# Performance work log

Hardware: AMD Instinct MI355X
Metric: run time of the kernel (lower is better)

Reference implementation:

```python
import jax, jax.numpy as jnp
import numpy as np

N, E, FN, FE, H, B = 8192, 32768, 32, 16, 73, 64
T_MP, T_S2S = 3, 12


def setup_inputs() -> dict:
    key = jax.random.key(0)
    k = jax.random.split(key, 24)
    s = 0.1
    p = lambda i, shape: jax.random.normal(k[i], shape, jnp.float32) * s
    return {
        "node_feats": jax.random.normal(k[0], (N, FN), jnp.float32),
        "edge_feats": jax.random.normal(k[1], (E, FE), jnp.float32),
        "W_in": p(2, (FN, H)), "b_in": p(3, (H,)),
        "ee_W1": p(4, (FE, H)), "ee_b1": p(5, (H,)),
        "ee_W2": p(6, (H, H * H)), "ee_b2": p(7, (H * H,)),
        "gru_Wih": p(8, (3 * H, H)), "gru_Whh": p(9, (3 * H, H)),
        "gru_bih": p(10, (3 * H,)), "gru_bhh": p(11, (3 * H,)),
        "lstm_Wih": p(12, (4 * H, 2 * H)), "lstm_Whh": p(13, (4 * H, H)),
        "lstm_bih": p(14, (4 * H,)), "lstm_bhh": p(15, (4 * H,)),
        "W_out": p(16, (H, 1)), "b_out": p(17, (1,)),
        "Esrc": jax.random.randint(k[18], (E,), 0, N),
        "Etgt": jax.random.randint(k[19], (E,), 0, N),
        "batch": jnp.sort(jax.random.randint(k[20], (N,), 0, B)),
    }


def reference(node_feats, edge_feats, W_in, b_in, ee_W1, ee_b1, ee_W2, ee_b2,
              gru_Wih, gru_Whh, gru_bih, gru_bhh,
              lstm_Wih, lstm_Whh, lstm_bih, lstm_bhh, W_out, b_out,
              Esrc, Etgt, batch):
    # EdgeEncoderMLP: edge features -> per-edge HxH weight matrices (Gilmer edge network)
    A = (jax.nn.relu(edge_feats @ ee_W1 + ee_b1) @ ee_W2 + ee_b2).reshape(E, H, H)
    h = node_feats @ W_in + b_in  # [N, H]

    def mp_step(h, _):
        m = jnp.einsum('eij,ej->ei', A, h[Esrc])           # per-edge matvec (gather-matmul)
        agg = jax.ops.segment_sum(m, Etgt, num_segments=N)  # scatter-add to targets
        # GRUCell update (torch gate order r,z,n)
        gi = agg @ gru_Wih.T + gru_bih
        gh = h @ gru_Whh.T + gru_bhh
        ir, iz, inn = jnp.split(gi, 3, axis=-1)
        hr, hz, hn = jnp.split(gh, 3, axis=-1)
        r = jax.nn.sigmoid(ir + hr)
        z = jax.nn.sigmoid(iz + hz)
        n = jnp.tanh(inn + r * hn)
        return (1.0 - z) * n + z * h, None

    h, _ = jax.lax.scan(mp_step, h, None, length=T_MP)

    # Set2Set pooling with a 1-layer LSTM (torch gate order i,f,g,o)
    def s2s_step(carry, _):
        q_star, hh, cc = carry
        gates = q_star @ lstm_Wih.T + lstm_bih + hh @ lstm_Whh.T + lstm_bhh
        i, f, g, o = jnp.split(gates, 4, axis=-1)
        cc = jax.nn.sigmoid(f) * cc + jax.nn.sigmoid(i) * jnp.tanh(g)
        hh = jax.nn.sigmoid(o) * jnp.tanh(cc)
        q = hh                                              # [B, H]
        e = jnp.sum(h * q[batch], axis=-1)                  # [N] attention logits
        emax = jax.ops.segment_max(e, batch, num_segments=B)
        a = jnp.exp(e - emax[batch])
        a = a / jax.ops.segment_sum(a, batch, num_segments=B)[batch]
        r = jax.ops.segment_sum(a[:, None] * h, batch, num_segments=B)
        return (jnp.concatenate([q, r], axis=-1), hh, cc), None

    init = (jnp.zeros((B, 2 * H), h.dtype), jnp.zeros((B, H), h.dtype),
            jnp.zeros((B, H), h.dtype))
    (q_star, _, _), _ = jax.lax.scan(s2s_step, init, None, length=T_S2S)
    return q_star[:, :H] @ W_out + b_out  # [B, 1]
```

## Files before the change

kernel.cpp:

```cpp
#include <hip/hip_runtime.h>

typedef _Float16 f16;
typedef f16 f16x2 __attribute__((ext_vector_type(2)));
typedef f16 f16x4 __attribute__((ext_vector_type(4)));
typedef f16 f16x8 __attribute__((ext_vector_type(8)));
typedef float f32x4 __attribute__((ext_vector_type(4)));

#define AS1 __attribute__((address_space(1)))
#define AS3 __attribute__((address_space(3)))

#define NN 8192
#define EE 32768

#if __has_builtin(__builtin_amdgcn_fdot2)
#define HAS_FDOT2 1
#else
#define HAS_FDOT2 0
#endif

__device__ __forceinline__ void glds16(const void* g, void* l) {
  __builtin_amdgcn_global_load_lds((const AS1 unsigned int*)g, (AS3 unsigned int*)l, 16, 0, 0);
}
__device__ __forceinline__ void stage_bytes(const void* g, void* s, int nbytes, int tid) {
  const int lane = tid & 63;
  for (int off = tid * 16; off < nbytes; off += 4096)
    glds16((const char*)g + off, (char*)s + (off - lane * 16));
}

__global__ void prep_kernel(
    const float* __restrict__ nf, const float* __restrict__ ef,
    const float* __restrict__ W_in, const float* __restrict__ b_in,
    const float* __restrict__ W1, const float* __restrict__ b1,
    const float* __restrict__ W2, const float* __restrict__ b2,
    const float* __restrict__ gWih, const float* __restrict__ gWhh,
    const float* __restrict__ lWih, const float* __restrict__ lWhh,
    const int* __restrict__ batch, const int* __restrict__ Etgt,
    float* __restrict__ h, f16* __restrict__ hf, f16* __restrict__ ehh,
    f16* __restrict__ W2f, f16* __restrict__ WihT, f16* __restrict__ WhhT,
    f16* __restrict__ Wcat, int* __restrict__ segstarts,
    int* __restrict__ count, int* __restrict__ bucket) {
  int t = blockIdx.x * 256 + threadIdx.x;
  if (t < 786432) {
    int n = t / 96, i = t - n * 96;
    float v = 0.f;
    if (i < 73) {
      v = b_in[i];
      const float* nr = nf + n * 32;
      #pragma unroll
      for (int f = 0; f < 32; ++f) v += nr[f] * W_in[f * 73 + i];
    }
    h[t] = v; hf[t] = (f16)v;
    return;
  }
  t -= 786432;
  if (t < 2621440) {
    int e = t / 80, k = t - e * 80;
    float v;
    if (k < 73) {
      v = b1[k];
      const float* er = ef + e * 16;
      #pragma unroll
      for (int f = 0; f < 16; ++f) v += er[f] * W1[f * 73 + k];
      v = fmaxf(v, 0.f);
    } else v = (k == 73) ? 1.f : 0.f;
    ehh[t] = (f16)v;
    return;
  }
  t -= 2621440;
  if (t < 614400) {
    int kg = t / 7680, r = t - kg * 7680;
    int nt = r / 1536, r2 = r - nt * 1536;
    int ks = r2 / 512, r3 = r2 - ks * 512;
    int l = r3 >> 3, j = r3 & 7;
    int mr = l & 15, q = l >> 4;
    int i = nt * 16 + mr, jj = ks * 32 + q * 8 + j;
    float v = 0.f;
    if (i < 73 && jj < 73) {
      if (kg < 73) v = W2[kg * 5329 + i * 73 + jj];
      else if (kg == 73) v = b2[i * 73 + jj];
    }
    W2f[t] = (f16)v;
    return;
  }
  t -= 614400;
  if (t < 43008) {
    int half = t / 21504, r = t - half * 21504;
    int g = r / 96, k = r - g * 96;
    float v = 0.f;
    if (g < 219 && k < 73) v = half ? gWhh[g * 73 + k] : gWih[g * 73 + k];
    (half ? WhhT : WihT)[r] = (f16)v;
    return;
  }
  t -= 43008;
  if (t < 67744) {
    int g = t / 232, k = t - g * 232;
    float v = 0.f;
    if (k < 73) v = lWih[g * 146 + k];
    else if (k >= 76 && k < 149) v = lWih[g * 146 + (k - 3)];
    else if (k >= 152 && k < 225) v = lWhh[g * 73 + (k - 152)];
    Wcat[t] = (f16)v;
    return;
  }
  t -= 67744;
  if (t < 65) {
    int key = t, lo = 0, hi = NN;
    while (lo < hi) { int mid = (lo + hi) >> 1; if (batch[mid] < key) lo = mid + 1; else hi = mid; }
    segstarts[t] = lo;
    return;
  }
  t -= 65;
  if (t < EE) {
    int tg = Etgt[t];
    int slot = atomicAdd(&count[tg], 1);
    if (slot < 64) bucket[tg * 64 + slot] = t;
  }
}

__global__ __launch_bounds__(256, 2) void vgemm_kernel(
    const f16* __restrict__ ehh, const f16* __restrict__ hf,
    const f16* __restrict__ W2f, const int* __restrict__ Esrc,
    f16* __restrict__ m) {
  __shared__ __align__(16) f16 w2s[2][15360];
  const int tid = threadIdx.x;
  const int bm = blockIdx.x & 127, ksp = blockIdx.x >> 7;
  const int e0 = bm * 256;
  const int kg0 = ksp * 20;
  const int wave = tid >> 6, lane = tid & 63;
  const int q = lane >> 4, mr = lane & 15;

  stage_bytes(W2f + kg0 * 7680, w2s[0], 30720, tid);

  f16x8 hsv[4][3];
  size_t er80[4];
  #pragma unroll
  for (int mt = 0; mt < 4; ++mt) {
    int er = e0 + wave * 64 + mt * 16 + mr;
    int srcn = Esrc[er];
    er80[mt] = (size_t)er * 80;
    #pragma unroll
    for (int ks = 0; ks < 3; ++ks)
      hsv[mt][ks] = *(const f16x8*)(hf + (size_t)srcn * 96 + ks * 32 + q * 8);
  }

  f32x4 zero = {0.f, 0.f, 0.f, 0.f};
  f32x4 acc[4][5];
  #pragma unroll
  for (int mt = 0; mt < 4; ++mt)
    #pragma unroll
    for (int nt = 0; nt < 5; ++nt) acc[mt][nt] = zero;

  for (int ch = 0; ch < 10; ++ch) {
    f16x2 evq[4];
    #pragma unroll
    for (int mt = 0; mt < 4; ++mt)
      evq[mt] = *(const f16x2*)(ehh + er80[mt] + kg0 + ch * 2);
    __syncthreads();
    if (ch + 1 < 10)
      stage_bytes(W2f + (kg0 + (ch + 1) * 2) * 7680, w2s[(ch + 1) & 1], 30720, tid);
    const f16* wb = w2s[ch & 1];
    #pragma unroll
    for (int i = 0; i < 2; ++i) {
      f16x8 af[4][3];
      #pragma unroll
      for (int mt = 0; mt < 4; ++mt) {
        f16 ev = evq[mt][i];
        f16x8 evv = {ev, ev, ev, ev, ev, ev, ev, ev};
        #pragma unroll
        for (int ks = 0; ks < 3; ++ks) af[mt][ks] = hsv[mt][ks] * evv;
      }
      const f16* wbi = wb + i * 7680;
      #pragma unroll
      for (int nt = 0; nt < 5; ++nt) {
        #pragma unroll
        for (int ks = 0; ks < 3; ++ks) {
          f16x8 bf = *(const f16x8*)(wbi + (nt * 3 + ks) * 512 + lane * 8);
          #pragma unroll
          for (int mt = 0; mt < 4; ++mt)
            acc[mt][nt] = __builtin_amdgcn_mfma_f32_16x16x32_f16(af[mt][ks], bf, acc[mt][nt], 0, 0, 0);
        }
      }
    }
  }
  #pragma unroll
  for (int mt = 0; mt < 4; ++mt) {
    #pragma unroll
    for (int reg = 0; reg < 4; ++reg) {
      int er = e0 + wave * 64 + mt * 16 + q * 4 + reg;
      f16* mp = m + (size_t)er * 320 + ksp * 80;
      #pragma unroll
      for (int nt = 0; nt < 5; ++nt)
        mp[nt * 16 + mr] = (f16)acc[mt][nt][reg];
    }
  }
}

__global__ void gather_kernel(const f16* __restrict__ m, const int* __restrict__ count,
                              const int* __restrict__ bucket, f16* __restrict__ aggf) {
  int t = blockIdx.x * 384 + threadIdx.x;
  int n = t / 96, i = t - n * 96;
  float s = 0.f;
  if (i < 80) {
    int cnt = count[n]; if (cnt > 64) cnt = 64;
    const int* bk = bucket + n * 64;
    for (int j = 0; j < cnt; ++j) {
      const f16* mp = m + (size_t)bk[j] * 320;
      s += ((float)mp[i] + (float)mp[80 + i]) + ((float)mp[160 + i] + (float)mp[240 + i]);
    }
  }
  aggf[t] = (f16)s;
}

__global__ __launch_bounds__(256, 1) void grugemm_kernel(
    const f16* __restrict__ aggf, const f16* __restrict__ hf,
    const f16* __restrict__ WihT, const f16* __restrict__ WhhT,
    f16* __restrict__ G) {
  __shared__ __align__(16) f16 As[128 * 96];
  __shared__ __align__(16) f16 Bs[224 * 96];
  const int tid = threadIdx.x;
  const int bz = blockIdx.x >> 6, bm = blockIdx.x & 63;
  const int m0 = bm * 128;
  const f16* A = bz ? hf : aggf;
  const f16* B = bz ? WhhT : WihT;
  f16* out = G + bz * (NN * 224);
  stage_bytes(A + m0 * 96, As, 128 * 96 * 2, tid);
  stage_bytes(B, Bs, 224 * 96 * 2, tid);
  const int wave = tid >> 6, lane = tid & 63, q = lane >> 4, mr = lane & 15;
  __syncthreads();
  f16x8 af[2][3];
  #pragma unroll
  for (int mt = 0; mt < 2; ++mt)
    #pragma unroll
    for (int ks = 0; ks < 3; ++ks)
      af[mt][ks] = *(const f16x8*)(As + (wave * 32 + mt * 16 + mr) * 96 + ks * 32 + q * 8);
  f32x4 zero = {0.f, 0.f, 0.f, 0.f};
  f32x4 acc[2][14];
  #pragma unroll
  for (int mt = 0; mt < 2; ++mt)
    #pragma unroll
    for (int nt = 0; nt < 14; ++nt) acc[mt][nt] = zero;
  #pragma unroll
  for (int nt = 0; nt < 14; ++nt) {
    #pragma unroll
    for (int ks = 0; ks < 3; ++ks) {
      f16x8 bf = *(const f16x8*)(Bs + (nt * 16 + mr) * 96 + ks * 32 + q * 8);
      #pragma unroll
      for (int mt = 0; mt < 2; ++mt)
        acc[mt][nt] = __builtin_amdgcn_mfma_f32_16x16x32_f16(af[mt][ks], bf, acc[mt][nt], 0, 0, 0);
    }
  }
  #pragma unroll
  for (int mt = 0; mt < 2; ++mt)
    #pragma unroll
    for (int reg = 0; reg < 4; ++reg) {
      int row = m0 + wave * 32 + mt * 16 + q * 4 + reg;
      #pragma unroll
      for (int nt = 0; nt < 14; ++nt)
        out[row * 224 + nt * 16 + mr] = (f16)acc[mt][nt][reg];
    }
}

__global__ void gate_kernel(const f16* __restrict__ G, const float* __restrict__ bih,
                            const float* __restrict__ bhh, float* __restrict__ h,
                            f16* __restrict__ hf) {
  int idx = blockIdx.x * 256 + threadIdx.x;
  int n = idx / 73, i = idx - n * 73;
  const f16* g0 = G + n * 224;
  const f16* g1 = G + NN * 224 + n * 224;
  float rr = (float)g0[i] + bih[i] + (float)g1[i] + bhh[i];
  rr = 1.f / (1.f + __expf(-rr));
  float zz = (float)g0[73 + i] + bih[73 + i] + (float)g1[73 + i] + bhh[73 + i];
  zz = 1.f / (1.f + __expf(-zz));
  float nx = (float)g0[146 + i] + bih[146 + i] + rr * ((float)g1[146 + i] + bhh[146 + i]);
  float nn_ = 2.f / (1.f + __expf(-2.f * nx)) - 1.f;
  float hv = h[n * 96 + i];
  float hn = (1.f - zz) * nn_ + zz * hv;
  h[n * 96 + i] = hn;
  hf[n * 96 + i] = (f16)hn;
}

__device__ __forceinline__ float wred_sum(float v) {
  #pragma unroll
  for (int off = 32; off; off >>= 1) v += __shfl_xor(v, off, 64);
  return v;
}
__device__ __forceinline__ float dot8(f16x8 w, f16x8 x, float acc) {
#if HAS_FDOT2
  acc = __builtin_amdgcn_fdot2((f16x2)__builtin_shufflevector(w, w, 0, 1),
                               (f16x2)__builtin_shufflevector(x, x, 0, 1), acc, false);
  acc = __builtin_amdgcn_fdot2((f16x2)__builtin_shufflevector(w, w, 2, 3),
                               (f16x2)__builtin_shufflevector(x, x, 2, 3), acc, false);
  acc = __builtin_amdgcn_fdot2((f16x2)__builtin_shufflevector(w, w, 4, 5),
                               (f16x2)__builtin_shufflevector(x, x, 4, 5), acc, false);
  acc = __builtin_amdgcn_fdot2((f16x2)__builtin_shufflevector(w, w, 6, 7),
                               (f16x2)__builtin_shufflevector(x, x, 6, 7), acc, false);
#else
  #pragma unroll
  for (int e = 0; e < 8; ++e) acc += (float)w[e] * (float)x[e];
#endif
  return acc;
}
__device__ __forceinline__ float dot4(f16x4 w, f16x4 x, float acc) {
#if HAS_FDOT2
  acc = __builtin_amdgcn_fdot2((f16x2)__builtin_shufflevector(w, w, 0, 1),
                               (f16x2)__builtin_shufflevector(x, x, 0, 1), acc, false);
  acc = __builtin_amdgcn_fdot2((f16x2)__builtin_shufflevector(w, w, 2, 3),
                               (f16x2)__builtin_shufflevector(x, x, 2, 3), acc, false);
#else
  #pragma unroll
  for (int e = 0; e < 4; ++e) acc += (float)w[e] * (float)x[e];
#endif
  return acc;
}

#define S2SCAP 256
#define NCAP 190

__global__ __launch_bounds__(512, 2) void s2s_kernel(
    const float* __restrict__ h, const f16* __restrict__ hf,
    const f16* __restrict__ Wcat,
    const float* __restrict__ lbih, const float* __restrict__ lbhh,
    const float* __restrict__ Wout, const float* __restrict__ bout,
    const int* __restrict__ segstarts, float* __restrict__ out) {
  __shared__ __align__(16) f16 hseg[NCAP * 84];
  __shared__ __align__(16) f16 xcat[240];
  __shared__ float hhv[80];
  __shared__ float gatesv[292];
  __shared__ float earr[S2SCAP];
  __shared__ float red[4];
  __shared__ __align__(16) float rpart[19 * 80];
  const int t = threadIdx.x, b = blockIdx.x;
  const int wid = t >> 6, lane = t & 63;

  const int s0 = segstarts[b];
  int segT = segstarts[b + 1] - s0;
  if (segT > S2SCAP) segT = S2SCAP;
  const int c = segT < NCAP ? segT : NCAP;

  if (t < 240) xcat[t] = (f16)0.f;
  if (t < 80) hhv[t] = 0.f;

  for (int r = wid; r < c; r += 8) {
    if (lane < 19) {
      f16x4 v = *(const f16x4*)(hf + (size_t)(s0 + r) * 96 + lane * 4);
      *(f16x4*)(hseg + r * 84 + lane * 4) = v;
    } else if (lane < 21) {
      f16x4 z = {(f16)0.f, (f16)0.f, (f16)0.f, (f16)0.f};
      *(f16x4*)(hseg + r * 84 + 76 + (lane - 19) * 4) = z;
    }
  }

  const bool isg = (t >= 220);
  const int g2 = t - 220;
  float bias = 0.f;
  if (isg) bias = lbih[g2] + lbhh[g2];
  f16x8 wihF[19], whhF[10];
  {
    const f16* wr = Wcat + (size_t)(isg ? g2 : 0) * 232;
    #pragma unroll
    for (int v = 0; v < 19; ++v) wihF[v] = *(const f16x8*)(wr + v * 8);
    #pragma unroll
    for (int v = 0; v < 10; ++v) whhF[v] = *(const f16x8*)(wr + 152 + v * 8);
  }
  const int nc = t / 10, fo = t - nc * 10;
  float creg = 0.f;
  __syncthreads();

  for (int iter = 0; iter < 12; ++iter) {
    if (isg) {
      float a0 = bias, a1 = 0.f, a2 = 0.f, a3 = 0.f;
      #pragma unroll
      for (int v = 0; v < 19; ++v) {
        f16x8 x = *(const f16x8*)(xcat + v * 8);
        int sel = v & 3;
        if (sel == 0) a0 = dot8(wihF[v], x, a0);
        else if (sel == 1) a1 = dot8(wihF[v], x, a1);
        else if (sel == 2) a2 = dot8(wihF[v], x, a2);
        else a3 = dot8(wihF[v], x, a3);
      }
      #pragma unroll
      for (int v = 0; v < 10; ++v) {
        f16x8 x = *(const f16x8*)(xcat + 152 + v * 8);
        int sel = v & 3;
        if (sel == 0) a0 = dot8(whhF[v], x, a0);
        else if (sel == 1) a1 = dot8(whhF[v], x, a1);
        else if (sel == 2) a2 = dot8(whhF[v], x, a2);
        else a3 = dot8(whhF[v], x, a3);
      }
      gatesv[g2] = (a0 + a1) + (a2 + a3);
    }
    __syncthreads();
    if (t < 73) {
      float ig = 1.f / (1.f + __expf(-gatesv[t]));
      float fg = 1.f / (1.f + __expf(-gatesv[73 + t]));
      float gx = gatesv[146 + t];
      float gg = 2.f / (1.f + __expf(-2.f * gx)) - 1.f;
      float og = 1.f / (1.f + __expf(-gatesv[219 + t]));
      creg = fg * creg + ig * gg;
      float cth = 2.f / (1.f + __expf(-2.f * creg)) - 1.f;
      float hh = og * cth;
      hhv[t] = hh;
      xcat[t] = (f16)hh;
      xcat[152 + t] = (f16)hh;
    }
    __syncthreads();
    if (wid < 3) {
      float a = 0.f;
      if (t < c) {
        const f16* hp = hseg + t * 84;
        float e0 = 0.f, e1 = 0.f;
        #pragma unroll
        for (int k = 0; k < 9; ++k) {
          f16x4 h0 = *(const f16x4*)(hp + 8 * k);
          f16x4 h1 = *(const f16x4*)(hp + 8 * k + 4);
          f16x4 x0 = *(const f16x4*)(xcat + 8 * k);
          f16x4 x1 = *(const f16x4*)(xcat + 8 * k + 4);
          e0 = dot4(h0, x0, e0);
          e1 = dot4(h1, x1, e1);
        }
        f16x4 ht = *(const f16x4*)(hp + 72);
        f16x4 xt = *(const f16x4*)(xcat + 72);
        e0 = dot4(ht, xt, e0);
        a = __expf(fminf(e0 + e1, 80.f));
        earr[t] = a;
      }
      float ws = wred_sum(a);
      if (lane == 0) red[wid] = ws;
    }
    if (wid == 0) {
      float fa = 0.f;
      int n = NCAP + lane;
      if (n < segT) {
        const float* hr = h + (size_t)(s0 + n) * 96;
        float e = 0.f;
        for (int i = 0; i < 73; ++i) e += hr[i] * hhv[i];
        fa = __expf(fminf(e, 80.f));
        earr[n] = fa;
      }
      float ws2 = wred_sum(fa);
      if (lane == 0) red[3] = ws2;
    }
    __syncthreads();
    if (t < 190) {
      float r0 = 0.f, r1 = 0.f, r2 = 0.f, r3 = 0.f, r4 = 0.f, r5 = 0.f, r6 = 0.f, r7 = 0.f;
      #pragma unroll
      for (int j = 0; j < 10; ++j) {
        int n = nc * 10 + j;
        if (n < c) {
          float a = earr[n];
          const f16* hp = hseg + n * 84 + fo * 8;
          f16x4 v0 = *(const f16x4*)(hp);
          f16x4 v1 = *(const f16x4*)(hp + 4);
          r0 += a * (float)v0[0]; r1 += a * (float)v0[1];
          r2 += a * (float)v0[2]; r3 += a * (float)v0[3];
          r4 += a * (float)v1[0]; r5 += a * (float)v1[1];
          r6 += a * (float)v1[2]; r7 += a * (float)v1[3];
        }
      }
      if (nc == 18) {
        for (int n = NCAP; n < segT; ++n) {
          float a = earr[n];
          const f16* hp = hf + (size_t)(s0 + n) * 96 + fo * 8;
          f16x4 v0 = *(const f16x4*)(hp);
          f16x4 v1 = *(const f16x4*)(hp + 4);
          r0 += a * (float)v0[0]; r1 += a * (float)v0[1];
          r2 += a * (float)v0[2]; r3 += a * (float)v0[3];
          r4 += a * (float)v1[0]; r5 += a * (float)v1[1];
          r6 += a * (float)v1[2]; r7 += a * (float)v1[3];
        }
      }
      f32x4 wa = {r0, r1, r2, r3}, wb = {r4, r5, r6, r7};
      *(f32x4*)(rpart + nc * 80 + fo * 8) = wa;
      *(f32x4*)(rpart + nc * 80 + fo * 8 + 4) = wb;
    }
    __syncthreads();
    if (t < 80) {
      float S = red[0] + red[1] + red[2] + red[3];
      float invS = (S > 0.f) ? (1.f / S) : 0.f;
      float r = 0.f;
      #pragma unroll
      for (int ch = 0; ch < 19; ++ch) r += rpart[ch * 80 + t];
      if (t < 73) xcat[76 + t] = (f16)(r * invS);
    }
    __syncthreads();
  }
  if (t < 80) gatesv[t] = (t < 73) ? hhv[t] * Wout[t] : 0.f;
  __syncthreads();
  if (t == 0) {
    float a = bout[0];
    for (int i = 0; i < 73; ++i) a += gatesv[i];
    out[b] = a;
  }
}

#define OFF_H      0u
#define OFF_G      3145728u
#define OFF_HF     17825792u
#define OFF_AGGF   19398656u
#define OFF_EHH    20971520u
#define OFF_W2F    26214400u
#define OFF_WIHT   27443200u
#define OFF_WHHT   27486208u
#define OFF_WCAT   27529216u
#define OFF_SEG    27664704u
#define OFF_CNT    27665024u
#define OFF_BKT    27697792u
#define OFF_M      29794944u

extern "C" void kernel_launch(void* const* d_in, const int* in_sizes, int n_in,
                              void* d_out, int out_size, void* d_ws, size_t ws_size,
                              hipStream_t stream) {
  const float* nf   = (const float*)d_in[0];
  const float* ef   = (const float*)d_in[1];
  const float* W_in = (const float*)d_in[2];
  const float* b_in = (const float*)d_in[3];
  const float* W1   = (const float*)d_in[4];
  const float* b1   = (const float*)d_in[5];
  const float* W2   = (const float*)d_in[6];
  const float* b2   = (const float*)d_in[7];
  const float* gWih = (const float*)d_in[8];
  const float* gWhh = (const float*)d_in[9];
  const float* gbih = (const float*)d_in[10];
  const float* gbhh = (const float*)d_in[11];
  const float* lWih = (const float*)d_in[12];
  const float* lWhh = (const float*)d_in[13];
  const float* lbih = (const float*)d_in[14];
  const float* lbhh = (const float*)d_in[15];
  const float* Wout = (const float*)d_in[16];
  const float* bout = (const float*)d_in[17];
  const int* Esrc   = (const int*)d_in[18];
  const int* Etgt   = (const int*)d_in[19];
  const int* batch  = (const int*)d_in[20];

  char* ws = (char*)d_ws;
  float* h    = (float*)(ws + OFF_H);
  f16* G      = (f16*)(ws + OFF_G);
  f16* m      = (f16*)(ws + OFF_M);
  f16* hf     = (f16*)(ws + OFF_HF);
  f16* aggf   = (f16*)(ws + OFF_AGGF);
  f16* ehh    = (f16*)(ws + OFF_EHH);
  f16* W2f    = (f16*)(ws + OFF_W2F);
  f16* WihT   = (f16*)(ws + OFF_WIHT);
  f16* WhhT   = (f16*)(ws + OFF_WHHT);
  f16* Wcat   = (f16*)(ws + OFF_WCAT);
  int* segst  = (int*)(ws + OFF_SEG);
  int* cnt    = (int*)(ws + OFF_CNT);
  int* bkt    = (int*)(ws + OFF_BKT);

  hipMemsetAsync(cnt, 0, NN * sizeof(int), stream);
  prep_kernel<<<16273, 256, 0, stream>>>(nf, ef, W_in, b_in, W1, b1, W2, b2,
                                         gWih, gWhh, lWih, lWhh, batch, Etgt,
                                         h, hf, ehh, W2f, WihT, WhhT, Wcat,
                                         segst, cnt, bkt);
  for (int step = 0; step < 3; ++step) {
    vgemm_kernel<<<512, 256, 0, stream>>>(ehh, hf, W2f, Esrc, m);
    gather_kernel<<<2048, 384, 0, stream>>>(m, cnt, bkt, aggf);
    grugemm_kernel<<<128, 256, 0, stream>>>(aggf, hf, WihT, WhhT, G);
    gate_kernel<<<2336, 256, 0, stream>>>(G, gbih, gbhh, h, hf);
  }
  s2s_kernel<<<64, 512, 0, stream>>>(h, hf, Wcat, lbih, lbhh, Wout, bout, segst,
                                     (float*)d_out);
}
```

Before: 331.8 us.

## Reassociate edge network: aggregate outer products per node before GEMM with W2

The per-edge matvec followed by scatter-add is reordered. Each node first sums the outer products of edge-encoder activations and source hidden states (pbuild), and a single GEMM of these per-node tensors against W2 (pgemm) then produces the aggregate directly. The GEMM dimension drops from edges to nodes, and the per-edge message buffer and gather pass go away. In exchange, a large per-node P tensor (N x 5632 fp16) must be written and read each step. Separately, the Set2Set LSTM folds Whh into Wih, since hh equals q_star's first half, and the attention loop pads to a fixed cap to drop a branch.

```diff
diff --git a/kernel.cpp b/kernel.cpp
--- a/kernel.cpp
+++ b/kernel.cpp
@@ -26,6 +26,8 @@
   for (int off = tid * 16; off < nbytes; off += 4096)
     glds16((const char*)g + off, (char*)s + (off - lane * 16));
 }
+
+#define KTOT 5632
 
 __global__ void prep_kernel(
     const float* __restrict__ nf, const float* __restrict__ ef,
@@ -36,7 +38,7 @@
     const float* __restrict__ lWih, const float* __restrict__ lWhh,
     const int* __restrict__ batch, const int* __restrict__ Etgt,
     float* __restrict__ h, f16* __restrict__ hf, f16* __restrict__ ehh,
-    f16* __restrict__ W2f, f16* __restrict__ WihT, f16* __restrict__ WhhT,
+    f16* __restrict__ W2p, f16* __restrict__ WihT, f16* __restrict__ WhhT,
     f16* __restrict__ Wcat, int* __restrict__ segstarts,
     int* __restrict__ count, int* __restrict__ bucket) {
   int t = blockIdx.x * 256 + threadIdx.x;
@@ -67,22 +69,22 @@
     return;
   }
   t -= 2621440;
-  if (t < 614400) {
-    int kg = t / 7680, r = t - kg * 7680;
-    int nt = r / 1536, r2 = r - nt * 1536;
-    int ks = r2 / 512, r3 = r2 - ks * 512;
-    int l = r3 >> 3, j = r3 & 7;
+  if (t < 450560) {
+    int c = t / 10240, r = t - c * 10240;
+    int kstep = r / 2560, r2 = r - kstep * 2560;
+    int nt = r2 / 512, r3 = r2 - nt * 512;
+    int l = r3 >> 3, idx = r3 & 7;
     int mr = l & 15, q = l >> 4;
-    int i = nt * 16 + mr, jj = ks * 32 + q * 8 + j;
+    int i = nt * 16 + mr;
+    int kk = c * 128 + kstep * 32 + q * 8 + idx;
+    int kg = kk / 76, j = kk - kg * 76;
     float v = 0.f;
-    if (i < 73 && jj < 73) {
-      if (kg < 73) v = W2[kg * 5329 + i * 73 + jj];
-      else if (kg == 73) v = b2[i * 73 + jj];
-    }
-    W2f[t] = (f16)v;
+    if (i < 73 && j < 73 && kg < 74)
+      v = (kg < 73) ? W2[kg * 5329 + i * 73 + j] : b2[i * 73 + j];
+    W2p[t] = (f16)v;
     return;
   }
-  t -= 614400;
+  t -= 450560;
   if (t < 43008) {
     int half = t / 21504, r = t - half * 21504;
     int g = r / 96, k = r - g * 96;
@@ -95,9 +97,8 @@
   if (t < 67744) {
     int g = t / 232, k = t - g * 232;
     float v = 0.f;
-    if (k < 73) v = lWih[g * 146 + k];
+    if (k < 73) v = lWih[g * 146 + k] + lWhh[g * 73 + k];
     else if (k >= 76 && k < 149) v = lWih[g * 146 + (k - 3)];
-    else if (k >= 152 && k < 225) v = lWhh[g * 73 + (k - 152)];
     Wcat[t] = (f16)v;
     return;
   }
@@ -116,98 +117,117 @@
   }
 }
 
-__global__ __launch_bounds__(256, 2) void vgemm_kernel(
+__global__ __launch_bounds__(256) void pbuild_kernel(
     const f16* __restrict__ ehh, const f16* __restrict__ hf,
-    const f16* __restrict__ W2f, const int* __restrict__ Esrc,
-    f16* __restrict__ m) {
-  __shared__ __align__(16) f16 w2s[2][15360];
+    const int* __restrict__ Esrc, const int* __restrict__ count,
+    const int* __restrict__ bucket, f16* __restrict__ P) {
+  const int wave = threadIdx.x >> 6, lane = threadIdx.x & 63;
+  const int n = blockIdx.x * 4 + wave;
+  int cnt = count[n]; if (cnt > 64) cnt = 64;
+  const int* bk = bucket + n * 64;
+  float acc[22][4];
+  #pragma unroll
+  for (int qi = 0; qi < 22; ++qi)
+    #pragma unroll
+    for (int x = 0; x < 4; ++x) acc[qi][x] = 0.f;
+  for (int s = 0; s < cnt; ++s) {
+    int e = bk[s];
+    const f16* er = ehh + (size_t)e * 80;
+    const f16* hr = hf + (size_t)Esrc[e] * 96;
+    #pragma unroll
+    for (int qi = 0; qi < 22; ++qi) {
+      int qd = lane + qi * 64;
+      if (qd < 1406) {
+        int kg = qd / 19, jq = qd - kg * 19;
+        float ev = (float)er[kg];
+        f16x4 hv = *(const f16x4*)(hr + jq * 4);
+        acc[qi][0] += ev * (float)hv[0];
+        acc[qi][1] += ev * (float)hv[1];
+        acc[qi][2] += ev * (float)hv[2];
+        acc[qi][3] += ev * (float)hv[3];
+      }
+    }
+  }
+  f16* pr = P + (size_t)n * KTOT;
+  #pragma unroll
+  for (int qi = 0; qi < 22; ++qi) {
+    f16x4 v = {(f16)acc[qi][0], (f16)acc[qi][1], (f16)acc[qi][2], (f16)acc[qi][3]};
+    *(f16x4*)(pr + (lane + qi * 64) * 4) = v;
+  }
+}
+
+__device__ __forceinline__ void stageA(const f16* __restrict__ P, int n0, int c,
+                                       f16* dst, int tid) {
+  const int lane = tid & 63;
+  #pragma unroll
+  for (int p = 0; p < 2; ++p) {
+    int off = tid * 16 + p * 4096;
+    int slot = off >> 4;
+    int kstep = slot >> 7, rem = slot & 127;
+    int mt = rem >> 6, l = rem & 63;
+    int r = mt * 16 + (l & 15);
+    int k = kstep * 32 + ((l >> 4) << 3);
+    glds16(P + (size_t)(n0 + r) * KTOT + c * 128 + k, (char*)dst + (off - lane * 16));
+  }
+}
+
+__global__ __launch_bounds__(256, 2) void pgemm_kernel(
+    const f16* __restrict__ P, const f16* __restrict__ W2p,
+    f16* __restrict__ aggf) {
+  __shared__ __align__(16) char smem[57344];
+  f16* As = (f16*)smem;
+  f16* Bs = (f16*)(smem + 16384);
+  float* red = (float*)smem;
   const int tid = threadIdx.x;
-  const int bm = blockIdx.x & 127, ksp = blockIdx.x >> 7;
-  const int e0 = bm * 256;
-  const int kg0 = ksp * 20;
-  const int wave = tid >> 6, lane = tid & 63;
+  const int lane = tid & 63, w = tid >> 6;
+  const int n0 = blockIdx.x * 32;
+
+  stageA(P, n0, 0, As, tid);
+  stage_bytes(W2p, Bs, 20480, tid);
+
+  f32x4 zero = {0.f, 0.f, 0.f, 0.f};
+  f32x4 acc[2][5];
+  #pragma unroll
+  for (int mt = 0; mt < 2; ++mt)
+    #pragma unroll
+    for (int nt = 0; nt < 5; ++nt) acc[mt][nt] = zero;
+
+  for (int c = 0; c < 44; ++c) {
+    __syncthreads();
+    if (c + 1 < 44) {
+      stageA(P, n0, c + 1, As + ((c + 1) & 1) * 4096, tid);
+      stage_bytes((const char*)W2p + (c + 1) * 20480, Bs + ((c + 1) & 1) * 10240, 20480, tid);
+    }
+    const f16* ab = As + (c & 1) * 4096;
+    const f16* bb = Bs + (c & 1) * 10240;
+    f16x8 af0 = *(const f16x8*)(ab + (w * 2 + 0) * 512 + lane * 8);
+    f16x8 af1 = *(const f16x8*)(ab + (w * 2 + 1) * 512 + lane * 8);
+    #pragma unroll
+    for (int nt = 0; nt < 5; ++nt) {
+      f16x8 bf = *(const f16x8*)(bb + (w * 5 + nt) * 512 + lane * 8);
+      acc[0][nt] = __builtin_amdgcn_mfma_f32_16x16x32_f16(af0, bf, acc[0][nt], 0, 0, 0);
+      acc[1][nt] = __builtin_amdgcn_mfma_f32_16x16x32_f16(af1, bf, acc[1][nt], 0, 0, 0);
+    }
+  }
+  __syncthreads();
   const int q = lane >> 4, mr = lane & 15;
-
-  stage_bytes(W2f + kg0 * 7680, w2s[0], 30720, tid);
-
-  f16x8 hsv[4][3];
-  size_t er80[4];
-  #pragma unroll
-  for (int mt = 0; mt < 4; ++mt) {
-    int er = e0 + wave * 64 + mt * 16 + mr;
-    int srcn = Esrc[er];
-    er80[mt] = (size_t)er * 80;
-    #pragma unroll
-    for (int ks = 0; ks < 3; ++ks)
-      hsv[mt][ks] = *(const f16x8*)(hf + (size_t)srcn * 96 + ks * 32 + q * 8);
-  }
-
-  f32x4 zero = {0.f, 0.f, 0.f, 0.f};
-  f32x4 acc[4][5];
-  #pragma unroll
-  for (int mt = 0; mt < 4; ++mt)
-    #pragma unroll
-    for (int nt = 0; nt < 5; ++nt) acc[mt][nt] = zero;
-
-  for (int ch = 0; ch < 10; ++ch) {
-    f16x2 evq[4];
-    #pragma unroll
-    for (int mt = 0; mt < 4; ++mt)
-      evq[mt] = *(const f16x2*)(ehh + er80[mt] + kg0 + ch * 2);
-    __syncthreads();
-    if (ch + 1 < 10)
-      stage_bytes(W2f + (kg0 + (ch + 1) * 2) * 7680, w2s[(ch + 1) & 1], 30720, tid);
-    const f16* wb = w2s[ch & 1];
-    #pragma unroll
-    for (int i = 0; i < 2; ++i) {
-      f16x8 af[4][3];
-      #pragma unroll
-      for (int mt = 0; mt < 4; ++mt) {
-        f16 ev = evq[mt][i];
-        f16x8 evv = {ev, ev, ev, ev, ev, ev, ev, ev};
-        #pragma unroll
-        for (int ks = 0; ks < 3; ++ks) af[mt][ks] = hsv[mt][ks] * evv;
-      }
-      const f16* wbi = wb + i * 7680;
-      #pragma unroll
-      for (int nt = 0; nt < 5; ++nt) {
-        #pragma unroll
-        for (int ks = 0; ks < 3; ++ks) {
-          f16x8 bf = *(const f16x8*)(wbi + (nt * 3 + ks) * 512 + lane * 8);
-          #pragma unroll
-          for (int mt = 0; mt < 4; ++mt)
-            acc[mt][nt] = __builtin_amdgcn_mfma_f32_16x16x32_f16(af[mt][ks], bf, acc[mt][nt], 0, 0, 0);
-        }
-      }
-    }
-  }
-  #pragma unroll
-  for (int mt = 0; mt < 4; ++mt) {
-    #pragma unroll
-    for (int reg = 0; reg < 4; ++reg) {
-      int er = e0 + wave * 64 + mt * 16 + q * 4 + reg;
-      f16* mp = m + (size_t)er * 320 + ksp * 80;
-      #pragma unroll
-      for (int nt = 0; nt < 5; ++nt)
-        mp[nt * 16 + mr] = (f16)acc[mt][nt][reg];
-    }
-  }
-}
-
-__global__ void gather_kernel(const f16* __restrict__ m, const int* __restrict__ count,
-                              const int* __restrict__ bucket, f16* __restrict__ aggf) {
-  int t = blockIdx.x * 384 + threadIdx.x;
-  int n = t / 96, i = t - n * 96;
-  float s = 0.f;
-  if (i < 80) {
-    int cnt = count[n]; if (cnt > 64) cnt = 64;
-    const int* bk = bucket + n * 64;
-    for (int j = 0; j < cnt; ++j) {
-      const f16* mp = m + (size_t)bk[j] * 320;
-      s += ((float)mp[i] + (float)mp[80 + i]) + ((float)mp[160 + i] + (float)mp[240 + i]);
-    }
-  }
-  aggf[t] = (f16)s;
+  #pragma unroll
+  for (int mt = 0; mt < 2; ++mt)
+    #pragma unroll
+    for (int nt = 0; nt < 5; ++nt)
+      #pragma unroll
+      for (int reg = 0; reg < 4; ++reg)
+        red[(w * 32 + mt * 16 + q * 4 + reg) * 80 + nt * 16 + mr] = acc[mt][nt][reg];
+  __syncthreads();
+  for (int idx = tid; idx < 3072; idx += 256) {
+    int row = idx / 96, i = idx - row * 96;
+    float s = 0.f;
+    if (i < 80) {
+      #pragma unroll
+      for (int ww = 0; ww < 4; ++ww) s += red[(ww * 32 + row) * 80 + i];
+    }
+    aggf[(size_t)(n0 + row) * 96 + i] = (f16)s;
+  }
 }
 
 __global__ __launch_bounds__(256, 1) void grugemm_kernel(
@@ -338,14 +358,14 @@
 
   if (t < 240) xcat[t] = (f16)0.f;
   if (t < 80) hhv[t] = 0.f;
-
-  for (int r = wid; r < c; r += 8) {
-    if (lane < 19) {
-      f16x4 v = *(const f16x4*)(hf + (size_t)(s0 + r) * 96 + lane * 4);
+  if (t < S2SCAP) earr[t] = 0.f;
+
+  for (int r = wid; r < NCAP; r += 8) {
+    if (lane < 21) {
+      f16x4 v = {(f16)0.f, (f16)0.f, (f16)0.f, (f16)0.f};
+      if (r < c && lane < 19)
+        v = *(const f16x4*)(hf + (size_t)(s0 + r) * 96 + lane * 4);
       *(f16x4*)(hseg + r * 84 + lane * 4) = v;
-    } else if (lane < 21) {
-      f16x4 z = {(f16)0.f, (f16)0.f, (f16)0.f, (f16)0.f};
-      *(f16x4*)(hseg + r * 84 + 76 + (lane - 19) * 4) = z;
     }
   }
 
@@ -353,13 +373,11 @@
   const int g2 = t - 220;
   float bias = 0.f;
   if (isg) bias = lbih[g2] + lbhh[g2];
-  f16x8 wihF[19], whhF[10];
+  f16x8 wihF[19];
   {
     const f16* wr = Wcat + (size_t)(isg ? g2 : 0) * 232;
     #pragma unroll
     for (int v = 0; v < 19; ++v) wihF[v] = *(const f16x8*)(wr + v * 8);
-    #pragma unroll
-    for (int v = 0; v < 10; ++v) whhF[v] = *(const f16x8*)(wr + 152 + v * 8);
   }
   const int nc = t / 10, fo = t - nc * 10;
   float creg = 0.f;
@@ -376,15 +394,6 @@
         else if (sel == 1) a1 = dot8(wihF[v], x, a1);
         else if (sel == 2) a2 = dot8(wihF[v], x, a2);
         else a3 = dot8(wihF[v], x, a3);
-      }
-      #pragma unroll
-      for (int v = 0; v < 10; ++v) {
-        f16x8 x = *(const f16x8*)(xcat + 152 + v * 8);
-        int sel = v & 3;
-        if (sel == 0) a0 = dot8(whhF[v], x, a0);
-        else if (sel == 1) a1 = dot8(whhF[v], x, a1);
-        else if (sel == 2) a2 = dot8(whhF[v], x, a2);
-        else a3 = dot8(whhF[v], x, a3);
       }
       gatesv[g2] = (a0 + a1) + (a2 + a3);
     }
@@ -400,7 +409,6 @@
       float hh = og * cth;
       hhv[t] = hh;
       xcat[t] = (f16)hh;
-      xcat[152 + t] = (f16)hh;
     }
     __syncthreads();
     if (wid < 3) {
@@ -445,16 +453,14 @@
       #pragma unroll
       for (int j = 0; j < 10; ++j) {
         int n = nc * 10 + j;
-        if (n < c) {
-          float a = earr[n];
-          const f16* hp = hseg + n * 84 + fo * 8;
-          f16x4 v0 = *(const f16x4*)(hp);
-          f16x4 v1 = *(const f16x4*)(hp + 4);
-          r0 += a * (float)v0[0]; r1 += a * (float)v0[1];
-          r2 += a * (float)v0[2]; r3 += a * (float)v0[3];
-          r4 += a * (float)v1[0]; r5 += a * (float)v1[1];
-          r6 += a * (float)v1[2]; r7 += a * (float)v1[3];
-        }
+        float a = earr[n];
+        const f16* hp = hseg + n * 84 + fo * 8;
+        f16x4 v0 = *(const f16x4*)(hp);
+        f16x4 v1 = *(const f16x4*)(hp + 4);
+        r0 += a * (float)v0[0]; r1 += a * (float)v0[1];
+        r2 += a * (float)v0[2]; r3 += a * (float)v0[3];
+        r4 += a * (float)v1[0]; r5 += a * (float)v1[1];
+        r6 += a * (float)v1[2]; r7 += a * (float)v1[3];
       }
       if (nc == 18) {
         for (int n = NCAP; n < segT; ++n) {
@@ -497,14 +503,14 @@
 #define OFF_HF     17825792u
 #define OFF_AGGF   19398656u
 #define OFF_EHH    20971520u
-#define OFF_W2F    26214400u
+#define OFF_W2P    26214400u
 #define OFF_WIHT   27443200u
 #define OFF_WHHT   27486208u
 #define OFF_WCAT   27529216u
 #define OFF_SEG    27664704u
 #define OFF_CNT    27665024u
 #define OFF_BKT    27697792u
-#define OFF_M      29794944u
+#define OFF_P      29794944u
 
 extern "C" void kernel_launch(void* const* d_in, const int* in_sizes, int n_in,
                               void* d_out, int out_size, void* d_ws, size_t ws_size,
@@ -534,11 +540,11 @@
   char* ws = (char*)d_ws;
   float* h    = (float*)(ws + OFF_H);
   f16* G      = (f16*)(ws + OFF_G);
-  f16* m      = (f16*)(ws + OFF_M);
+  f16* P      = (f16*)(ws + OFF_P);
   f16* hf     = (f16*)(ws + OFF_HF);
   f16* aggf   = (f16*)(ws + OFF_AGGF);
   f16* ehh    = (f16*)(ws + OFF_EHH);
-  f16* W2f    = (f16*)(ws + OFF_W2F);
+  f16* W2p    = (f16*)(ws + OFF_W2P);
   f16* WihT   = (f16*)(ws + OFF_WIHT);
   f16* WhhT   = (f16*)(ws + OFF_WHHT);
   f16* Wcat   = (f16*)(ws + OFF_WCAT);
@@ -547,13 +553,13 @@
   int* bkt    = (int*)(ws + OFF_BKT);
 
   hipMemsetAsync(cnt, 0, NN * sizeof(int), stream);
-  prep_kernel<<<16273, 256, 0, stream>>>(nf, ef, W_in, b_in, W1, b1, W2, b2,
+  prep_kernel<<<15634, 256, 0, stream>>>(nf, ef, W_in, b_in, W1, b1, W2, b2,
                                          gWih, gWhh, lWih, lWhh, batch, Etgt,
-                                         h, hf, ehh, W2f, WihT, WhhT, Wcat,
+                                         h, hf, ehh, W2p, WihT, WhhT, Wcat,
                                          segst, cnt, bkt);
   for (int step = 0; step < 3; ++step) {
-    vgemm_kernel<<<512, 256, 0, stream>>>(ehh, hf, W2f, Esrc, m);
-    gather_kernel<<<2048, 384, 0, stream>>>(m, cnt, bkt, aggf);
+    pbuild_kernel<<<2048, 256, 0, stream>>>(ehh, hf, Esrc, cnt, bkt, P);
+    pgemm_kernel<<<256, 256, 0, stream>>>(P, W2p, aggf);
     grugemm_kernel<<<128, 256, 0, stream>>>(aggf, hf, WihT, WhhT, G);
     gate_kernel<<<2336, 256, 0, stream>>>(G, gbih, gbhh, h, hf);
   }
```

Result: slower. 473.1 us (+42.6%).

## Fuse aggregation, GRU GEMM and gate into one kernel; fold LSTM Whh into Wih

Applied to the files above, without the earlier changes.

Three per-step kernels (neighbor gather, GRU GEMM and gate) are merged into a single kernel. Each 32-node block sums its incoming messages into shared memory, runs the MFMA GEMMs against WihT and WhhT, keeps the gate pre-activations in shared memory, and applies the GRU update in place. This removes the global round trips for aggf and G and two launches per step. The cost is far fewer threads doing the latency-bound gather (256 blocks versus 2048), so its parallelism drops. In Set2Set, q equals the LSTM hidden state, so lstm_Whh is added into the first block of lstm_Wih to drop one matvec, and zero-padding the node tile removes per-row bounds checks.

```diff
diff --git a/kernel.cpp b/kernel.cpp
--- a/kernel.cpp
+++ b/kernel.cpp
@@ -95,9 +95,8 @@
   if (t < 67744) {
     int g = t / 232, k = t - g * 232;
     float v = 0.f;
-    if (k < 73) v = lWih[g * 146 + k];
+    if (k < 73) v = lWih[g * 146 + k] + lWhh[g * 73 + k];
     else if (k >= 76 && k < 149) v = lWih[g * 146 + (k - 3)];
-    else if (k >= 152 && k < 225) v = lWhh[g * 73 + (k - 152)];
     Wcat[t] = (f16)v;
     return;
   }
@@ -194,88 +193,76 @@
   }
 }
 
-__global__ void gather_kernel(const f16* __restrict__ m, const int* __restrict__ count,
-                              const int* __restrict__ bucket, f16* __restrict__ aggf) {
-  int t = blockIdx.x * 384 + threadIdx.x;
-  int n = t / 96, i = t - n * 96;
-  float s = 0.f;
-  if (i < 80) {
-    int cnt = count[n]; if (cnt > 64) cnt = 64;
-    const int* bk = bucket + n * 64;
+__global__ __launch_bounds__(256, 2) void aggru_kernel(
+    const f16* __restrict__ m, const int* __restrict__ count,
+    const int* __restrict__ bucket, const f16* __restrict__ WihT,
+    const f16* __restrict__ WhhT, const float* __restrict__ bih,
+    const float* __restrict__ bhh, float* __restrict__ h, f16* __restrict__ hf) {
+  __shared__ __align__(16) f16 Hs[32 * 96];
+  __shared__ __align__(16) f16 As[32 * 96];
+  __shared__ __align__(16) f16 Gs[2][32][224];
+  const int tid = threadIdx.x;
+  const int n0 = blockIdx.x * 32;
+
+  stage_bytes(hf + (size_t)n0 * 96, Hs, 6144, tid);
+  {
+    int n = tid >> 3, j = tid & 7;
+    f16x2 z = {(f16)0.f, (f16)0.f};
+    *(f16x2*)(As + n * 96 + 80 + j * 2) = z;
+  }
+  #pragma unroll
+  for (int k = 0; k < 10; ++k) {
+    int o = tid + k * 256;
+    int n = o / 80, i = o - n * 80;
+    int cnt = count[n0 + n]; if (cnt > 64) cnt = 64;
+    const int* bk = bucket + (size_t)(n0 + n) * 64;
+    float s = 0.f;
     for (int j = 0; j < cnt; ++j) {
       const f16* mp = m + (size_t)bk[j] * 320;
       s += ((float)mp[i] + (float)mp[80 + i]) + ((float)mp[160 + i] + (float)mp[240 + i]);
     }
-  }
-  aggf[t] = (f16)s;
-}
-
-__global__ __launch_bounds__(256, 1) void grugemm_kernel(
-    const f16* __restrict__ aggf, const f16* __restrict__ hf,
-    const f16* __restrict__ WihT, const f16* __restrict__ WhhT,
-    f16* __restrict__ G) {
-  __shared__ __align__(16) f16 As[128 * 96];
-  __shared__ __align__(16) f16 Bs[224 * 96];
-  const int tid = threadIdx.x;
-  const int bz = blockIdx.x >> 6, bm = blockIdx.x & 63;
-  const int m0 = bm * 128;
-  const f16* A = bz ? hf : aggf;
-  const f16* B = bz ? WhhT : WihT;
-  f16* out = G + bz * (NN * 224);
-  stage_bytes(A + m0 * 96, As, 128 * 96 * 2, tid);
-  stage_bytes(B, Bs, 224 * 96 * 2, tid);
-  const int wave = tid >> 6, lane = tid & 63, q = lane >> 4, mr = lane & 15;
+    As[n * 96 + i] = (f16)s;
+  }
   __syncthreads();
-  f16x8 af[2][3];
-  #pragma unroll
-  for (int mt = 0; mt < 2; ++mt)
-    #pragma unroll
-    for (int ks = 0; ks < 3; ++ks)
-      af[mt][ks] = *(const f16x8*)(As + (wave * 32 + mt * 16 + mr) * 96 + ks * 32 + q * 8);
-  f32x4 zero = {0.f, 0.f, 0.f, 0.f};
-  f32x4 acc[2][14];
-  #pragma unroll
-  for (int mt = 0; mt < 2; ++mt)
-    #pragma unroll
-    for (int nt = 0; nt < 14; ++nt) acc[mt][nt] = zero;
+  const int w = tid >> 6, lane = tid & 63, q = lane >> 4, mr = lane & 15;
+  const int g = w & 1, mt = w >> 1;
+  const f16* Asrc = g ? Hs : As;
+  const f16* B = g ? WhhT : WihT;
+  f16x8 af[3];
+  #pragma unroll
+  for (int ks = 0; ks < 3; ++ks)
+    af[ks] = *(const f16x8*)(Asrc + (mt * 16 + mr) * 96 + ks * 32 + q * 8);
   #pragma unroll
   for (int nt = 0; nt < 14; ++nt) {
+    f32x4 acc = {0.f, 0.f, 0.f, 0.f};
     #pragma unroll
     for (int ks = 0; ks < 3; ++ks) {
-      f16x8 bf = *(const f16x8*)(Bs + (nt * 16 + mr) * 96 + ks * 32 + q * 8);
-      #pragma unroll
-      for (int mt = 0; mt < 2; ++mt)
-        acc[mt][nt] = __builtin_amdgcn_mfma_f32_16x16x32_f16(af[mt][ks], bf, acc[mt][nt], 0, 0, 0);
-    }
-  }
-  #pragma unroll
-  for (int mt = 0; mt < 2; ++mt)
-    #pragma unroll
-    for (int reg = 0; reg < 4; ++reg) {
-      int row = m0 + wave * 32 + mt * 16 + q * 4 + reg;
-      #pragma unroll
-      for (int nt = 0; nt < 14; ++nt)
-        out[row * 224 + nt * 16 + mr] = (f16)acc[mt][nt][reg];
-    }
-}
-
-__global__ void gate_kernel(const f16* __restrict__ G, const float* __restrict__ bih,
-                            const float* __restrict__ bhh, float* __restrict__ h,
-                            f16* __restrict__ hf) {
-  int idx = blockIdx.x * 256 + threadIdx.x;
-  int n = idx / 73, i = idx - n * 73;
-  const f16* g0 = G + n * 224;
-  const f16* g1 = G + NN * 224 + n * 224;
-  float rr = (float)g0[i] + bih[i] + (float)g1[i] + bhh[i];
-  rr = 1.f / (1.f + __expf(-rr));
-  float zz = (float)g0[73 + i] + bih[73 + i] + (float)g1[73 + i] + bhh[73 + i];
-  zz = 1.f / (1.f + __expf(-zz));
-  float nx = (float)g0[146 + i] + bih[146 + i] + rr * ((float)g1[146 + i] + bhh[146 + i]);
-  float nn_ = 2.f / (1.f + __expf(-2.f * nx)) - 1.f;
-  float hv = h[n * 96 + i];
-  float hn = (1.f - zz) * nn_ + zz * hv;
-  h[n * 96 + i] = hn;
-  hf[n * 96 + i] = (f16)hn;
+      f16x8 bf = *(const f16x8*)(B + (nt * 16 + mr) * 96 + ks * 32 + q * 8);
+      acc = __builtin_amdgcn_mfma_f32_16x16x32_f16(af[ks], bf, acc, 0, 0, 0);
+    }
+    #pragma unroll
+    for (int reg = 0; reg < 4; ++reg)
+      Gs[g][mt * 16 + q * 4 + reg][nt * 16 + mr] = (f16)acc[reg];
+  }
+  __syncthreads();
+  #pragma unroll
+  for (int k = 0; k < 10; ++k) {
+    int idx = tid + k * 256;
+    if (idx < 2336) {
+      int n = idx / 73, i = idx - n * 73;
+      float rr = (float)Gs[0][n][i] + bih[i] + (float)Gs[1][n][i] + bhh[i];
+      rr = 1.f / (1.f + __expf(-rr));
+      float zz = (float)Gs[0][n][73 + i] + bih[73 + i] + (float)Gs[1][n][73 + i] + bhh[73 + i];
+      zz = 1.f / (1.f + __expf(-zz));
+      float nx = (float)Gs[0][n][146 + i] + bih[146 + i] + rr * ((float)Gs[1][n][146 + i] + bhh[146 + i]);
+      float nn_ = 2.f / (1.f + __expf(-2.f * nx)) - 1.f;
+      size_t hi_ = (size_t)(n0 + n) * 96 + i;
+      float hv = h[hi_];
+      float hn = (1.f - zz) * nn_ + zz * hv;
+      h[hi_] = hn;
+      hf[hi_] = (f16)hn;
+    }
+  }
 }
 
 __device__ __forceinline__ float wred_sum(float v) {
@@ -338,14 +325,14 @@
 
   if (t < 240) xcat[t] = (f16)0.f;
   if (t < 80) hhv[t] = 0.f;
-
-  for (int r = wid; r < c; r += 8) {
-    if (lane < 19) {
-      f16x4 v = *(const f16x4*)(hf + (size_t)(s0 + r) * 96 + lane * 4);
+  if (t < S2SCAP) earr[t] = 0.f;
+
+  for (int r = wid; r < NCAP; r += 8) {
+    if (lane < 21) {
+      f16x4 v = {(f16)0.f, (f16)0.f, (f16)0.f, (f16)0.f};
+      if (r < c && lane < 19)
+        v = *(const f16x4*)(hf + (size_t)(s0 + r) * 96 + lane * 4);
       *(f16x4*)(hseg + r * 84 + lane * 4) = v;
-    } else if (lane < 21) {
-      f16x4 z = {(f16)0.f, (f16)0.f, (f16)0.f, (f16)0.f};
-      *(f16x4*)(hseg + r * 84 + 76 + (lane - 19) * 4) = z;
     }
   }
 
@@ -353,13 +340,11 @@
   const int g2 = t - 220;
   float bias = 0.f;
   if (isg) bias = lbih[g2] + lbhh[g2];
-  f16x8 wihF[19], whhF[10];
+  f16x8 wihF[19];
   {
     const f16* wr = Wcat + (size_t)(isg ? g2 : 0) * 232;
     #pragma unroll
     for (int v = 0; v < 19; ++v) wihF[v] = *(const f16x8*)(wr + v * 8);
-    #pragma unroll
-    for (int v = 0; v < 10; ++v) whhF[v] = *(const f16x8*)(wr + 152 + v * 8);
   }
   const int nc = t / 10, fo = t - nc * 10;
   float creg = 0.f;
@@ -376,15 +361,6 @@
         else if (sel == 1) a1 = dot8(wihF[v], x, a1);
         else if (sel == 2) a2 = dot8(wihF[v], x, a2);
         else a3 = dot8(wihF[v], x, a3);
-      }
-      #pragma unroll
-      for (int v = 0; v < 10; ++v) {
-        f16x8 x = *(const f16x8*)(xcat + 152 + v * 8);
-        int sel = v & 3;
-        if (sel == 0) a0 = dot8(whhF[v], x, a0);
-        else if (sel == 1) a1 = dot8(whhF[v], x, a1);
-        else if (sel == 2) a2 = dot8(whhF[v], x, a2);
-        else a3 = dot8(whhF[v], x, a3);
       }
       gatesv[g2] = (a0 + a1) + (a2 + a3);
     }
@@ -400,7 +376,6 @@
       float hh = og * cth;
       hhv[t] = hh;
       xcat[t] = (f16)hh;
-      xcat[152 + t] = (f16)hh;
     }
     __syncthreads();
     if (wid < 3) {
@@ -445,16 +420,14 @@
       #pragma unroll
       for (int j = 0; j < 10; ++j) {
         int n = nc * 10 + j;
-        if (n < c) {
-          float a = earr[n];
-          const f16* hp = hseg + n * 84 + fo * 8;
-          f16x4 v0 = *(const f16x4*)(hp);
-          f16x4 v1 = *(const f16x4*)(hp + 4);
-          r0 += a * (float)v0[0]; r1 += a * (float)v0[1];
-          r2 += a * (float)v0[2]; r3 += a * (float)v0[3];
-          r4 += a * (float)v1[0]; r5 += a * (float)v1[1];
-          r6 += a * (float)v1[2]; r7 += a * (float)v1[3];
-        }
+        float a = earr[n];
+        const f16* hp = hseg + n * 84 + fo * 8;
+        f16x4 v0 = *(const f16x4*)(hp);
+        f16x4 v1 = *(const f16x4*)(hp + 4);
+        r0 += a * (float)v0[0]; r1 += a * (float)v0[1];
+        r2 += a * (float)v0[2]; r3 += a * (float)v0[3];
+        r4 += a * (float)v1[0]; r5 += a * (float)v1[1];
+        r6 += a * (float)v1[2]; r7 += a * (float)v1[3];
       }
       if (nc == 18) {
         for (int n = NCAP; n < segT; ++n) {
@@ -493,9 +466,7 @@
 }
 
 #define OFF_H      0u
-#define OFF_G      3145728u
 #define OFF_HF     17825792u
-#define OFF_AGGF   19398656u
 #define OFF_EHH    20971520u
 #define OFF_W2F    26214400u
 #define OFF_WIHT   27443200u
@@ -533,10 +504,7 @@
 
   char* ws = (char*)d_ws;
   float* h    = (float*)(ws + OFF_H);
-  f16* G      = (f16*)(ws + OFF_G);
-  f16* m      = (f16*)(ws + OFF_M);
   f16* hf     = (f16*)(ws + OFF_HF);
-  f16* aggf   = (f16*)(ws + OFF_AGGF);
   f16* ehh    = (f16*)(ws + OFF_EHH);
   f16* W2f    = (f16*)(ws + OFF_W2F);
   f16* WihT   = (f16*)(ws + OFF_WIHT);
@@ -545,6 +513,7 @@
   int* segst  = (int*)(ws + OFF_SEG);
   int* cnt    = (int*)(ws + OFF_CNT);
   int* bkt    = (int*)(ws + OFF_BKT);
+  f16* m      = (f16*)(ws + OFF_M);
 
   hipMemsetAsync(cnt, 0, NN * sizeof(int), stream);
   prep_kernel<<<16273, 256, 0, stream>>>(nf, ef, W_in, b_in, W1, b1, W2, b2,
@@ -553,9 +522,7 @@
                                          segst, cnt, bkt);
   for (int step = 0; step < 3; ++step) {
     vgemm_kernel<<<512, 256, 0, stream>>>(ehh, hf, W2f, Esrc, m);
-    gather_kernel<<<2048, 384, 0, stream>>>(m, cnt, bkt, aggf);
-    grugemm_kernel<<<128, 256, 0, stream>>>(aggf, hf, WihT, WhhT, G);
-    gate_kernel<<<2336, 256, 0, stream>>>(G, gbih, gbhh, h, hf);
+    aggru_kernel<<<256, 256, 0, stream>>>(m, cnt, bkt, WihT, WhhT, gbih, gbhh, h, hf);
   }
   s2s_kernel<<<64, 512, 0, stream>>>(h, hf, Wcat, lbih, lbhh, Wout, bout, segst,
                                      (float*)d_out);
```

Result: slower. 374.4 us (+12.8%).
